# Optimization experiments

Hardware: AMD Instinct MI355X
Metric: run time of the kernel (lower is better)

Reference implementation:

```python
import jax, jax.numpy as jnp
from jax import lax
import numpy as np

DN = ('NCHW', 'OIHW', 'NCHW')
LEAKY_SLOPE = 0.01  # torch nn.LeakyReLU default


def conv(x, w, b=None, stride=1, pad=0):
    y = lax.conv_general_dilated(x, w, (stride, stride), [(pad, pad), (pad, pad)],
                                 dimension_numbers=DN)
    return y if b is None else y + b[None, :, None, None]


def conv_transpose2d(x, w, b):
    # torch ConvTranspose2d(k=4, s=2, p=1); w layout (Cin, Cout, 4, 4)
    wf = jnp.transpose(jnp.flip(w, (2, 3)), (1, 0, 2, 3))  # -> OIHW
    y = lax.conv_general_dilated(x, wf, (1, 1), [(2, 2), (2, 2)],
                                 lhs_dilation=(2, 2), dimension_numbers=DN)
    return y + b[None, :, None, None]


def residual_stack(x, rw3, rw1):
    # 6 ResidualLayers: x + conv1x1(relu(conv3x3(x))), both convs bias-free
    for i in range(rw3.shape[0]):
        h = jax.nn.relu(conv(x, rw3[i], pad=1))
        x = x + conv(h, rw1[i])
    return x


def vector_quantize(latents, codebook):
    # latents: [B, D, H, W] -> NHWC
    lat = jnp.transpose(latents, (0, 2, 3, 1))
    B, H, W, D = lat.shape
    flat = lat.reshape(-1, D)  # [N, D]
    # pairwise squared distances [N, K]
    dist = (jnp.sum(flat ** 2, axis=1, keepdims=True)
            + jnp.sum(codebook ** 2, axis=1)
            - 2.0 * flat @ codebook.T)
    inds = jnp.argmin(dist, axis=1)            # [N]
    q = codebook[inds].reshape(B, H, W, D)     # gather == one-hot matmul
    commitment_loss = jnp.mean((lax.stop_gradient(q) - lat) ** 2)
    embedding_loss = jnp.mean((q - lax.stop_gradient(lat)) ** 2)
    q_st = lat + lax.stop_gradient(q - lat)    # straight-through
    return jnp.transpose(q_st, (0, 3, 1, 2)), embedding_loss, commitment_loss


def setup_inputs() -> dict:
    key = jax.random.key(0)
    ks = iter(jax.random.split(key, 32))
    B, C, S = 16, 3, 128
    H0, H1 = 128, 256          # hidden_dims
    D, K = 64, 512             # embedding_dim, num_embeddings
    n_res = 6

    def w(shape, scale=0.05):
        return (jax.random.normal(next(ks), shape, dtype=jnp.float32) * scale)

    inp = {
        'x': jax.random.normal(next(ks), (B, C, S, S), dtype=jnp.float32),
        # encoder
        'ew0': w((H0, C, 4, 4)), 'eb0': jnp.zeros((H0,), jnp.float32),
        'ew1': w((H1, H0, 4, 4)), 'eb1': jnp.zeros((H1,), jnp.float32),
        'ew2': w((H1, H1, 3, 3)), 'eb2': jnp.zeros((H1,), jnp.float32),
        'erw3': w((n_res, H1, H1, 3, 3)),
        'erw1': w((n_res, H1, H1, 1, 1)),
        'ew3': w((D, H1, 1, 1)), 'eb3': jnp.zeros((D,), jnp.float32),
        # codebook, uniform(-1/K, 1/K) as in torch init
        'codebook': jax.random.uniform(next(ks), (K, D), jnp.float32, -1.0 / K, 1.0 / K),
        # decoder
        'dw0': w((H1, D, 3, 3)), 'db0': jnp.zeros((H1,), jnp.float32),
        'drw3': w((n_res, H1, H1, 3, 3)),
        'drw1': w((n_res, H1, H1, 1, 1)),
        'tw0': w((H1, H0, 4, 4)), 'tb0': jnp.zeros((H0,), jnp.float32),
        'tw1': w((H0, C, 4, 4)), 'tb1': jnp.zeros((C,), jnp.float32),
    }
    return inp


def reference(x, ew0, eb0, ew1, eb1, ew2, eb2, erw3, erw1, ew3, eb3,
              codebook, dw0, db0, drw3, drw1, tw0, tb0, tw1, tb1):
    lrelu = lambda t: jax.nn.leaky_relu(t, LEAKY_SLOPE)
    # encoder: two stride-2 downsamples, conv3x3, 6 residuals, 1x1 -> D
    h = lrelu(conv(x, ew0, eb0, stride=2, pad=1))   # [B,128,64,64]
    h = lrelu(conv(h, ew1, eb1, stride=2, pad=1))   # [B,256,32,32]
    h = lrelu(conv(h, ew2, eb2, stride=1, pad=1))
    h = residual_stack(h, erw3, erw1)
    h = lrelu(h)
    z = lrelu(conv(h, ew3, eb3))                    # [B,64,32,32]
    # vector quantization
    q, embedding_loss, commitment_loss = vector_quantize(z, codebook)
    # decoder
    d = lrelu(conv(q, dw0, db0, stride=1, pad=1))   # [B,256,32,32]
    d = residual_stack(d, drw3, drw1)
    d = lrelu(d)
    d = lrelu(conv_transpose2d(d, tw0, tb0))        # [B,128,64,64]
    recons = jnp.tanh(conv_transpose2d(d, tw1, tb1))  # [B,3,128,128]
    return recons, embedding_loss, commitment_loss
```

## Files before the change

kernel.cpp:

```cpp
#include <hip/hip_runtime.h>
#include <math.h>


typedef __attribute__((ext_vector_type(8))) short bf16x8;
typedef __attribute__((ext_vector_type(4))) float f32x4;

__device__ __forceinline__ float bf2f(short s) {
    unsigned u = ((unsigned)(unsigned short)s) << 16;
    return __builtin_bit_cast(float, u);
}
__device__ __forceinline__ unsigned short f2bfu(float f) {
    unsigned u = __builtin_bit_cast(unsigned, f);
    u = (u + 0x7fff + ((u >> 16) & 1)) >> 16;
    return (unsigned short)u;
}
__device__ __forceinline__ short f2bf(float f) { return (short)f2bfu(f); }
__device__ __forceinline__ int pack2(float a, float b) {
    return (int)f2bfu(a) | ((int)f2bfu(b) << 16);
}

template<int ACT>
__device__ __forceinline__ float actf(float v) {
    if (ACT == 1) return fmaxf(v, 0.f);
    if (ACT == 2) return v > 0.f ? v : 0.01f * v;
    return v;
}

__device__ __forceinline__ void gload_lds16(const void* g, void* l) {
    __builtin_amdgcn_global_load_lds(
        (const __attribute__((address_space(1))) unsigned int*)g,
        (__attribute__((address_space(3))) unsigned int*)l, 16, 0, 0);
}

__device__ __forceinline__ int fof(int r) { return (r & 3) ^ ((r >> 2) & 3); }

#define WAITV(N) asm volatile("s_waitcnt vmcnt(" #N ")" ::: "memory")
#define LGKM0 asm volatile("s_waitcnt lgkmcnt(0)" ::: "memory")

__global__ __launch_bounds__(256) void prep_perm_k(const float* __restrict__ src,
        short* __restrict__ dst, int COUT, int CIN, int T, int total) {
    int i = blockIdx.x * 256 + threadIdx.x;
    if (i >= total) return;
    int ic = i % CIN; int r = i / CIN;
    int oc = r % COUT; r /= COUT;
    int t = r % T; int c = r / T;
    dst[i] = f2bf(src[(((size_t)c * COUT + oc) * CIN + ic) * T + t]);
}

__global__ __launch_bounds__(256) void prep_tw0_k(const float* __restrict__ src,
        short* __restrict__ dst) {
    int i = blockIdx.x * 256 + threadIdx.x;
    if (i >= 4 * 4 * 128 * 256) return;
    int ic = i & 255; int r = i >> 8;
    int oc = r & 127; r >>= 7;
    int tap = r & 3; int par = r >> 2;
    int py = par >> 1, px = par & 1, my = tap >> 1, mx = tap & 1;
    int ky = 2 * my + (py ^ 1), kx = 2 * mx + (px ^ 1);
    dst[i] = f2bf(src[(((size_t)ic * 128 + oc) * 4 + ky) * 4 + kx]);
}

__global__ __launch_bounds__(256) void halo_zero_k(short* __restrict__ p,
        int W, int C) {
    int row = blockIdx.x, img = blockIdx.y;
    short* base = p + ((size_t)img * W + row) * W * C;
    bool full = (row < 2) || (row >= W - 2);
    int n = full ? W * C : 4 * C;
    for (int t = threadIdx.x * 8; t < n; t += 256 * 8) {
        int off = t;
        if (!full) off = (t < 2 * C) ? t : (W - 2) * C + (t - 2 * C);
        *(int4*)(base + off) = int4{0, 0, 0, 0};
    }
}

template<int CIN, int NTAPS, int TAPPAT, int SM, int INW, int OUTACT,
         bool HASB, bool FUSE>
__global__ __launch_bounds__(512, 1) void rconv_k(
        const short* __restrict__ in, const short* __restrict__ Wp,
        const float* __restrict__ bias, const short* __restrict__ W1p,
        short* __restrict__ outp) {
    constexpr int CH64 = (CIN >= 128) ? CIN / 64 : 1;
    constexpr int LG2 = (CH64 == 4) ? 2 : (CH64 == 2) ? 1 : 0;
    constexpr int ST = NTAPS * CH64;
    __shared__ short sLds[FUSE ? 81920 : 61440];
    const int tid = threadIdx.x;
    const int lane = tid & 63, wv = tid >> 6;
    const int wc = wv & 3, kg = wv >> 2;
    const int pix0 = blockIdx.x * 64;
    const int l15 = lane & 15, hi = lane >> 4;
    const int sl = (hi ^ fof(l15)) * 8;

    const int arow = (tid >> 2) & 63, akk = tid >> 8, aslot = tid & 3;
    const short* Aptr;
    {
        int pixa = pix0 + arow;
        int ba = pixa >> 10, Ya = (pixa >> 5) & 31, Xa = pixa & 31;
        Aptr = in + (size_t)((ba * INW + SM * Ya + 2) * INW + (SM * Xa + 2)) * CIN
                  + akk * 32 + (aslot ^ fof(arow)) * 8;
    }
    const short* Bptr[4];
#pragma unroll
    for (int j = 0; j < 4; j++) {
        int gb = tid + 512 * j;
        int kkb = gb >> 10, oc = (gb >> 2) & 255, slb = gb & 3;
        Bptr[j] = Wp + (size_t)oc * CIN + kkb * 32 + ((slb ^ fof(oc)) * 8);
    }

    auto stage = [&](int s, int bi) {
        int t = s >> LG2;
        int c0 = (s & (CH64 - 1)) * 64;
        int rof, cof;
        if (TAPPAT == 1) { rof = t / 3 - 1; cof = t % 3 - 1; }
        else             { rof = (t >> 2) - 1; cof = (t & 3) - 1; }
        int aoff = (rof * INW + cof) * CIN + c0;
        int woff = t * (256 * CIN) + c0;
        char* L = (char*)sLds + bi * 40960;
        gload_lds16(Aptr + aoff, L + tid * 16);
#pragma unroll
        for (int j = 0; j < 4; j++)
            gload_lds16(Bptr[j] + woff, L + 8192 + (tid + 512 * j) * 16);
    };

    f32x4 acc[4][4];
#pragma unroll
    for (int mi = 0; mi < 4; mi++)
#pragma unroll
        for (int ni = 0; ni < 4; ni++) acc[mi][ni] = f32x4{0.f, 0.f, 0.f, 0.f};

    stage(0, 0);
    stage(1, 1);
    int bi = 0;
    for (int s = 0; s < ST; ++s) {
        if (s < ST - 1) { WAITV(5); } else { WAITV(0); }
        __builtin_amdgcn_s_barrier();
        int nx = bi + 2; if (nx >= 3) nx -= 3;
        if (s + 2 < ST) stage(s + 2, nx);
        const short* LA = sLds + bi * 20480 + kg * 2048;
        const short* LB = sLds + bi * 20480 + 4096 + kg * 8192;
        bf16x8 af[4], bfr[4];
#pragma unroll
        for (int mi = 0; mi < 4; mi++)
            af[mi] = *(const bf16x8*)(LA + (mi * 16 + l15) * 32 + sl);
#pragma unroll
        for (int ni = 0; ni < 4; ni++)
            bfr[ni] = *(const bf16x8*)(LB + (wc * 64 + ni * 16 + l15) * 32 + sl);
        __builtin_amdgcn_s_setprio(1);
#pragma unroll
        for (int mi = 0; mi < 4; mi++)
#pragma unroll
            for (int ni = 0; ni < 4; ni++)
                acc[mi][ni] = __builtin_amdgcn_mfma_f32_16x16x32_bf16(
                    af[mi], bfr[ni], acc[mi][ni], 0, 0, 0);
        __builtin_amdgcn_s_setprio(0);
        bi = (bi == 2) ? 0 : bi + 1;
    }

    float* MB = (float*)sLds;

    const short* W1ptr[4];
    if (FUSE) {
#pragma unroll
        for (int j = 0; j < 4; j++) {
            int gb = tid + 512 * j;
            int kkb = gb >> 10, oc = (gb >> 2) & 255, slb = gb & 3;
            W1ptr[j] = W1p + (size_t)oc * 256 + kkb * 32 + ((slb ^ fof(oc)) * 8);
        }
    }
    auto stage2 = [&](int c) {
        char* L = (char*)sLds + 65536 + (c & 1) * 32768;
#pragma unroll
        for (int j = 0; j < 4; j++)
            gload_lds16(W1ptr[j] + c * 64, L + (tid + 512 * j) * 16);
    };

    __syncthreads();
    if (FUSE) { stage2(0); stage2(1); }
    if (kg == 1) {
#pragma unroll
        for (int mi = 0; mi < 4; mi++)
#pragma unroll
            for (int ni = 0; ni < 4; ni++)
#pragma unroll
                for (int r = 0; r < 4; r++)
                    MB[(mi * 16 + hi * 4 + r) * 256 + wc * 64 + ni * 16 + l15]
                        = acc[mi][ni][r];
    }
    __syncthreads();

    if (!FUSE) {
        if (kg == 0) {
#pragma unroll
            for (int mi = 0; mi < 4; mi++)
#pragma unroll
                for (int ni = 0; ni < 4; ni++) {
                    int col = wc * 64 + ni * 16 + l15;
                    float b = HASB ? bias[col] : 0.f;
#pragma unroll
                    for (int r = 0; r < 4; r++) {
                        int row = mi * 16 + hi * 4 + r;
                        MB[row * 256 + col] += acc[mi][ni][r] + b;
                    }
                }
        }
        __syncthreads();
#pragma unroll
        for (int j = 0; j < 4; j++) {
            int idx = j * 512 + tid;
            int p = idx >> 5, c0 = (idx & 31) * 8;
            int pix = pix0 + p;
            int b = pix >> 10, Y = (pix >> 5) & 31, X = pix & 31;
            size_t base = (((size_t)b * 36 + Y + 2) * 36 + X + 2) * 256 + c0;
            const float4* m4 = (const float4*)(MB + idx * 8);
            float4 lo = m4[0], hv = m4[1];
            int pk[4];
            pk[0] = pack2(actf<OUTACT>(lo.x), actf<OUTACT>(lo.y));
            pk[1] = pack2(actf<OUTACT>(lo.z), actf<OUTACT>(lo.w));
            pk[2] = pack2(actf<OUTACT>(hv.x), actf<OUTACT>(hv.y));
            pk[3] = pack2(actf<OUTACT>(hv.z), actf<OUTACT>(hv.w));
            *(int4*)(outp + base) = *(int4*)pk;
        }
        return;
    }

    short* H = sLds + 65536;
    if (kg == 0) {
#pragma unroll
        for (int mi = 0; mi < 4; mi++)
#pragma unroll
            for (int ni = 0; ni < 4; ni++) {
                int col = wc * 64 + ni * 16 + l15;
#pragma unroll
                for (int r = 0; r < 4; r++) {
                    int row = mi * 16 + hi * 4 + r;
                    float v = acc[mi][ni][r] + MB[row * 256 + col];
                    H[((col >> 5) * 64 + row) * 32
                      + (((col >> 3) & 3) ^ fof(row)) * 8 + (col & 7)]
                        = f2bf(fmaxf(v, 0.f));
                }
            }
    }
    __syncthreads();

    f32x4 acc2[4][4];
#pragma unroll
    for (int mi = 0; mi < 4; mi++)
#pragma unroll
        for (int ni = 0; ni < 4; ni++) acc2[mi][ni] = f32x4{0.f, 0.f, 0.f, 0.f};

    for (int s2 = 0; s2 < 4; ++s2) {
        if (s2 < 3) { WAITV(4); } else { WAITV(0); }
        __builtin_amdgcn_s_barrier();
        const short* HB = H + (s2 * 2 + kg) * 2048;
        const short* LW = sLds + 32768 + (s2 & 1) * 16384 + kg * 8192;
        bf16x8 af2[4], bf2r[4];
#pragma unroll
        for (int mi = 0; mi < 4; mi++)
            af2[mi] = *(const bf16x8*)(HB + (mi * 16 + l15) * 32 + sl);
#pragma unroll
        for (int ni = 0; ni < 4; ni++)
            bf2r[ni] = *(const bf16x8*)(LW + (wc * 64 + ni * 16 + l15) * 32 + sl);
        LGKM0;
        __builtin_amdgcn_sched_barrier(0);
        __builtin_amdgcn_s_barrier();
        if (s2 < 2) stage2(s2 + 2);
        __builtin_amdgcn_s_setprio(1);
#pragma unroll
        for (int mi = 0; mi < 4; mi++)
#pragma unroll
            for (int ni = 0; ni < 4; ni++)
                acc2[mi][ni] = __builtin_amdgcn_mfma_f32_16x16x32_bf16(
                    af2[mi], bf2r[ni], acc2[mi][ni], 0, 0, 0);
        __builtin_amdgcn_s_setprio(0);
    }

    __syncthreads();
    if (kg == 1) {
#pragma unroll
        for (int mi = 0; mi < 4; mi++)
#pragma unroll
            for (int ni = 0; ni < 4; ni++)
#pragma unroll
                for (int r = 0; r < 4; r++)
                    MB[(mi * 16 + hi * 4 + r) * 256 + wc * 64 + ni * 16 + l15]
                        = acc2[mi][ni][r];
    }
    __syncthreads();
    if (kg == 0) {
#pragma unroll
        for (int mi = 0; mi < 4; mi++)
#pragma unroll
            for (int ni = 0; ni < 4; ni++) {
                int col = wc * 64 + ni * 16 + l15;
#pragma unroll
                for (int r = 0; r < 4; r++) {
                    int row = mi * 16 + hi * 4 + r;
                    MB[row * 256 + col] += acc2[mi][ni][r];
                }
            }
    }
    __syncthreads();
#pragma unroll
    for (int j = 0; j < 4; j++) {
        int idx = j * 512 + tid;
        int p = idx >> 5, c0 = (idx & 31) * 8;
        int pix = pix0 + p;
        int b = pix >> 10, Y = (pix >> 5) & 31, X = pix & 31;
        size_t base = (((size_t)b * 36 + Y + 2) * 36 + X + 2) * 256 + c0;
        const float4* m4 = (const float4*)(MB + idx * 8);
        float4 lo = m4[0], hv = m4[1];
        bf16x8 rv = *(const bf16x8*)(in + base);
        int pk[4];
        pk[0] = pack2(actf<OUTACT>(lo.x + bf2f(rv[0])),
                      actf<OUTACT>(lo.y + bf2f(rv[1])));
        pk[1] = pack2(actf<OUTACT>(lo.z + bf2f(rv[2])),
                      actf<OUTACT>(lo.w + bf2f(rv[3])));
        pk[2] = pack2(actf<OUTACT>(hv.x + bf2f(rv[4])),
                      actf<OUTACT>(hv.y + bf2f(rv[5])));
        pk[3] = pack2(actf<OUTACT>(hv.z + bf2f(rv[6])),
                      actf<OUTACT>(hv.w + bf2f(rv[7])));
        *(int4*)(outp + base) = *(int4*)pk;
    }
}

template<int CIN, int COUT, int NTAPS, int TAPPAT, int SM, int INW,
         int OUTACT, bool RES, bool HASB, int OUTMODE, int BN>
__global__ __launch_bounds__(256) void gconv_k(
        const short* __restrict__ in, const short* __restrict__ Wp,
        const float* __restrict__ bias, const short* __restrict__ res,
        void* __restrict__ outp) {
    constexpr int KCH = CIN / 32;
    constexpr int LG = (KCH == 8) ? 3 : (KCH == 4) ? 2 : (KCH == 2) ? 1 : 0;
    constexpr int ST = NTAPS * KCH;
    constexpr int NF = BN / 32;
    constexpr int WN = BN / 2;
    __shared__ short sA[3 * 128 * 32];
    __shared__ short sB[3 * BN * 32];
    const int tid = threadIdx.x;
    const int lane = tid & 63, wv = tid >> 6;
    const int wr = wv >> 1, wc = wv & 1;
    const int pix0 = blockIdx.x * 128;
    const int oc0 = blockIdx.y * BN;
    int py = 0, px = 0;
    if (TAPPAT == 3) {
        int par = blockIdx.z;
        py = par >> 1; px = par & 1;
        Wp += (size_t)par * NTAPS * COUT * CIN;
    }
    const int sp = tid >> 2;
    const int swz = ((tid & 3) ^ fof(sp)) * 8;
    int rbA[2];
#pragma unroll
    for (int rd = 0; rd < 2; rd++) {
        int pix = pix0 + sp + rd * 64;
        int b = pix >> 10, Y = (pix >> 5) & 31, X = pix & 31;
        rbA[rd] = ((b * INW + SM * Y + 2) * INW + (SM * X + 2)) * CIN + swz;
    }
    const int wb0 = (oc0 + sp) * CIN + swz;
    const int wb1 = (oc0 + sp + 64) * CIN + swz;

    f32x4 acc[4][NF];
#pragma unroll
    for (int i = 0; i < 4; i++)
#pragma unroll
        for (int j = 0; j < NF; j++) acc[i][j] = f32x4{0.f, 0.f, 0.f, 0.f};

    const int sslot = ((lane >> 4) ^ fof(lane & 15)) * 8;
    const int abase = (wr * 64 + (lane & 15)) * 32 + sslot;
    const int bbase = (wc * WN + (lane & 15)) * 32 + sslot;

    auto stage = [&](int s, int biq) {
        int t = s >> LG, c = s & (KCH - 1);
        int rof, cof;
        if (TAPPAT == 0) { rof = 0; cof = 0; }
        else if (TAPPAT == 1) { rof = t / 3 - 1; cof = t % 3 - 1; }
        else if (TAPPAT == 2) { rof = t / 4 - 1; cof = t % 4 - 1; }
        else { int my = t >> 1, mx = t & 1;
               rof = (py == 0) ? -my : 1 - my;
               cof = (px == 0) ? -mx : 1 - mx; }
        const int tapoff = (rof * INW + cof) * CIN + c * 32;
        char* a = (char*)sA + biq * 8192;
        char* b = (char*)sB + biq * (BN * 64);
        const short* wt = Wp + (size_t)t * COUT * CIN + c * 32;
        gload_lds16(in + rbA[0] + tapoff, a + tid * 16);
        gload_lds16(in + rbA[1] + tapoff, a + 4096 + tid * 16);
        gload_lds16(wt + wb0, b + tid * 16);
        if (BN == 128) gload_lds16(wt + wb1, b + 4096 + tid * 16);
    };

    stage(0, 0);
    stage(1, 1);
    int cur = 0;
    for (int s = 0; s < ST; ++s) {
        if (s < ST - 1) {
            if (BN == 128) { WAITV(4); } else { WAITV(3); }
        } else {
            WAITV(0);
        }
        __builtin_amdgcn_s_barrier();
        int nxt = cur + 2; if (nxt >= 3) nxt -= 3;
        if (s + 2 < ST) stage(s + 2, nxt);
        const short* a = sA + cur * 4096;
        const short* b = sB + cur * (BN * 32);
        bf16x8 af[4], bfm[NF];
#pragma unroll
        for (int mi = 0; mi < 4; mi++)
            af[mi] = *(const bf16x8*)(a + abase + mi * 512);
#pragma unroll
        for (int ni = 0; ni < NF; ni++)
            bfm[ni] = *(const bf16x8*)(b + bbase + ni * 512);
        __builtin_amdgcn_s_setprio(1);
#pragma unroll
        for (int mi = 0; mi < 4; mi++)
#pragma unroll
            for (int ni = 0; ni < NF; ni++)
                acc[mi][ni] = __builtin_amdgcn_mfma_f32_16x16x32_bf16(
                    af[mi], bfm[ni], acc[mi][ni], 0, 0, 0);
        __builtin_amdgcn_s_setprio(0);
        cur = (cur == 2) ? 0 : cur + 1;
    }
#pragma unroll
    for (int mi = 0; mi < 4; mi++) {
#pragma unroll
        for (int r = 0; r < 4; r++) {
            int pix = pix0 + wr * 64 + mi * 16 + (lane >> 4) * 4 + r;
            int b = pix >> 10, Y = (pix >> 5) & 31, X = pix & 31;
            size_t rowoff = 0;
            if (OUTMODE == 0)
                rowoff = (((size_t)b * 36 + Y + 2) * 36 + X + 2) * COUT;
            else if (OUTMODE == 2)
                rowoff = (((size_t)b * 68 + 2 * Y + py + 2) * 68 + 2 * X + px + 2) * 128;
#pragma unroll
            for (int ni = 0; ni < NF; ni++) {
                int col = oc0 + wc * WN + ni * 16 + (lane & 15);
                float v = acc[mi][ni][r];
                if (HASB) v += bias[col];
                if (OUTMODE == 1) {
                    ((float*)outp)[(size_t)pix * COUT + col] = actf<OUTACT>(v);
                } else {
                    size_t off = rowoff + col;
                    if (RES) v += bf2f(res[off]);
                    ((short*)outp)[off] = f2bf(actf<OUTACT>(v));
                }
            }
        }
    }
}

__global__ __launch_bounds__(256) void conv0_k(const float* __restrict__ x,
        const float* __restrict__ W, const float* __restrict__ bias,
        short* __restrict__ P0) {
    __shared__ float sIn[3 * 4 * 130];
    __shared__ float sW[48 * 4 * 36];
    int y = blockIdx.x, b = blockIdx.y;
    int tid = threadIdx.x;
    for (int t = tid; t < 6144; t += 256) {
        int k = t >> 7, oc = t & 127;
        sW[(k * 4 + (oc >> 5)) * 36 + (oc & 31)] = W[(size_t)oc * 48 + k];
    }
    for (int t = tid; t < 1560; t += 256) {
        int ic = t / 520; int rem = t - ic * 520;
        int ry = rem / 130, rx = rem - ry * 130;
        int iy = 2 * y - 1 + ry, ix = rx - 1;
        float v = 0.f;
        if ((unsigned)iy < 128u && (unsigned)ix < 128u)
            v = x[((size_t)b * 3 + ic) * 16384 + iy * 128 + ix];
        sIn[t] = v;
    }
    __syncthreads();
    int p = tid >> 2, g = tid & 3, oc0 = g * 32;
    float acc[32];
#pragma unroll
    for (int o = 0; o < 32; o++) acc[o] = bias[oc0 + o];
#pragma unroll
    for (int ic = 0; ic < 3; ic++)
#pragma unroll
        for (int ky = 0; ky < 4; ky++) {
            const float* ib = sIn + ic * 520 + ky * 130 + 2 * p;
#pragma unroll
            for (int kx = 0; kx < 4; kx++) {
                float xv = ib[kx];
                const float* wr_ = sW + ((ic * 16 + ky * 4 + kx) * 4 + g) * 36;
#pragma unroll
                for (int q = 0; q < 8; q++) {
                    float4 w = *(const float4*)(wr_ + q * 4);
                    acc[4 * q + 0] += w.x * xv; acc[4 * q + 1] += w.y * xv;
                    acc[4 * q + 2] += w.z * xv; acc[4 * q + 3] += w.w * xv;
                }
            }
        }
    size_t base = (((size_t)b * 68 + y + 2) * 68 + p + 2) * 128 + oc0;
#pragma unroll
    for (int q4 = 0; q4 < 4; q4++) {
        int pk[4];
#pragma unroll
        for (int j = 0; j < 4; j++) {
            float v0 = actf<2>(acc[q4 * 8 + 2 * j]);
            float v1 = actf<2>(acc[q4 * 8 + 2 * j + 1]);
            pk[j] = pack2(v0, v1);
        }
        *(int4*)(P0 + base + q4 * 8) = *(int4*)pk;
    }
}

__global__ __launch_bounds__(256) void vq_argmin_k(const float* __restrict__ zr,
        const float* __restrict__ cb, int* __restrict__ ind) {
    __shared__ short sZ[2][128 * 32];
    __shared__ short sC[2][128 * 32];
    __shared__ float sN[128];
    const int tid = threadIdx.x;
    const int lane = tid & 63, wv = tid >> 6;
    const int pos0 = blockIdx.x * 128;
#pragma unroll
    for (int it = 0; it < 4; ++it) {
        int task = tid + it * 256;
        int row = task >> 3, kq = task & 7;
        const float4* zp = (const float4*)(zr + (size_t)(pos0 + row) * 64 + kq * 8);
        float4 v0 = zp[0], v1 = zp[1];
        int slot = ((kq & 3) ^ fof(row)) * 8;
        short tmp[8] = {f2bf(v0.x), f2bf(v0.y), f2bf(v0.z), f2bf(v0.w),
                        f2bf(v1.x), f2bf(v1.y), f2bf(v1.z), f2bf(v1.w)};
        *(bf16x8*)&sZ[kq >> 2][row * 32 + slot] = *(bf16x8*)tmp;
    }
    const int sslot = ((lane >> 4) ^ fof(lane & 15)) * 8;
    const int l15 = lane & 15;
    float best[2][4]; int bidx[2][4];
#pragma unroll
    for (int mi = 0; mi < 2; mi++)
#pragma unroll
        for (int r = 0; r < 4; r++) { best[mi][r] = INFINITY; bidx[mi][r] = 0; }
    for (int ch = 0; ch < 4; ++ch) {
        __syncthreads();
#pragma unroll
        for (int it = 0; it < 4; ++it) {
            int task = tid + it * 256;
            int row = task >> 3, kq = task & 7;
            const float4* cp = (const float4*)(cb + (size_t)(ch * 128 + row) * 64 + kq * 8);
            float4 v0 = cp[0], v1 = cp[1];
            int slot = ((kq & 3) ^ fof(row)) * 8;
            short tmp[8] = {f2bf(v0.x), f2bf(v0.y), f2bf(v0.z), f2bf(v0.w),
                            f2bf(v1.x), f2bf(v1.y), f2bf(v1.z), f2bf(v1.w)};
            *(bf16x8*)&sC[kq >> 2][row * 32 + slot] = *(bf16x8*)tmp;
        }
        if (tid < 128) {
            const float4* cp = (const float4*)(cb + (size_t)(ch * 128 + tid) * 64);
            float s = 0.f;
#pragma unroll
            for (int q = 0; q < 16; q++) {
                float4 v = cp[q];
                s += v.x * v.x + v.y * v.y + v.z * v.z + v.w * v.w;
            }
            sN[tid] = s;
        }
        __syncthreads();
        f32x4 acc[2][8];
#pragma unroll
        for (int mi = 0; mi < 2; mi++)
#pragma unroll
            for (int ni = 0; ni < 8; ni++) acc[mi][ni] = f32x4{0.f, 0.f, 0.f, 0.f};
#pragma unroll
        for (int kc = 0; kc < 2; ++kc) {
            bf16x8 za[2], ca[8];
#pragma unroll
            for (int mi = 0; mi < 2; mi++)
                za[mi] = *(const bf16x8*)&sZ[kc][(wv * 32 + mi * 16 + l15) * 32 + sslot];
#pragma unroll
            for (int ni = 0; ni < 8; ni++)
                ca[ni] = *(const bf16x8*)&sC[kc][(ni * 16 + l15) * 32 + sslot];
#pragma unroll
            for (int mi = 0; mi < 2; mi++)
#pragma unroll
                for (int ni = 0; ni < 8; ni++)
                    acc[mi][ni] = __builtin_amdgcn_mfma_f32_16x16x32_bf16(
                        za[mi], ca[ni], acc[mi][ni], 0, 0, 0);
        }
#pragma unroll
        for (int mi = 0; mi < 2; mi++)
#pragma unroll
            for (int ni = 0; ni < 8; ni++) {
                float nrm = sN[ni * 16 + l15];
                int idx = ch * 128 + ni * 16 + l15;
#pragma unroll
                for (int r = 0; r < 4; r++) {
                    float sc = nrm - 2.f * acc[mi][ni][r];
                    if (sc < best[mi][r]) { best[mi][r] = sc; bidx[mi][r] = idx; }
                }
            }
    }
#pragma unroll
    for (int m = 1; m < 16; m <<= 1) {
#pragma unroll
        for (int mi = 0; mi < 2; mi++)
#pragma unroll
            for (int r = 0; r < 4; r++) {
                float os = __shfl_xor(best[mi][r], m);
                int   oi = __shfl_xor(bidx[mi][r], m);
                if (os < best[mi][r] || (os == best[mi][r] && oi < bidx[mi][r])) {
                    best[mi][r] = os; bidx[mi][r] = oi;
                }
            }
    }
    if (l15 == 0) {
        int g = lane >> 4;
#pragma unroll
        for (int mi = 0; mi < 2; mi++)
#pragma unroll
            for (int r = 0; r < 4; r++)
                ind[pos0 + wv * 32 + mi * 16 + g * 4 + r] = bidx[mi][r];
    }
}

__global__ __launch_bounds__(256) void vq_gather_k(const float* __restrict__ zr,
        const float* __restrict__ cb, const int* __restrict__ ind,
        short* __restrict__ q, float* __restrict__ part) {
    int pos = blockIdx.x * 256 + threadIdx.x;
    int b = pos >> 10, hw = pos & 1023, y = hw >> 5, xx = hw & 31;
    int idx = ind[pos];
    const float4* cp = (const float4*)(cb + (size_t)idx * 64);
    const float4* zp = (const float4*)(zr + (size_t)pos * 64);
    size_t qb = (((size_t)b * 36 + y + 2) * 36 + xx + 2) * 64;
    float sum = 0.f;
#pragma unroll
    for (int d4 = 0; d4 < 16; d4++) {
        float4 c = cp[d4], z = zp[d4];
        float dx = c.x - z.x, dy = c.y - z.y, dz = c.z - z.z, dw = c.w - z.w;
        sum += dx * dx + dy * dy + dz * dz + dw * dw;
        ((int*)(q + qb))[2 * d4] = pack2(c.x, c.y);
        ((int*)(q + qb))[2 * d4 + 1] = pack2(c.z, c.w);
    }
#pragma unroll
    for (int m = 1; m < 64; m <<= 1) sum += __shfl_xor(sum, m);
    __shared__ float sred[4];
    int lane = threadIdx.x & 63, wvv = threadIdx.x >> 6;
    if (lane == 0) sred[wvv] = sum;
    __syncthreads();
    if (threadIdx.x == 0)
        part[blockIdx.x] = sred[0] + sred[1] + sred[2] + sred[3];
}

__global__ void finalize_k(const float* __restrict__ part, float* __restrict__ out) {
    if (threadIdx.x == 0) {
        float s = 0.f;
        for (int k = 0; k < 64; k++) s += part[k];
        float m = s / 1048576.f;
        out[786432] = m;
        out[786433] = m;
    }
}

__global__ __launch_bounds__(256) void tw1_k(const short* __restrict__ in,
        const float* __restrict__ W, const float* __restrict__ bias,
        float* __restrict__ out) {
    __shared__ float sW[16 * 128 * 4];
    int b = blockIdx.y, y0 = blockIdx.x * 8;
    int tid = threadIdx.x;
    for (int t = tid; t < 2048; t += 256) {
        int k = t >> 7, ic = t & 127;
        float4 v;
        v.x = W[((size_t)ic * 3 + 0) * 16 + k];
        v.y = W[((size_t)ic * 3 + 1) * 16 + k];
        v.z = W[((size_t)ic * 3 + 2) * 16 + k];
        v.w = 0.f;
        *(float4*)&sW[t * 4] = v;
    }
    __syncthreads();
    int r = tid >> 5, g = tid & 31;
    int oy = y0 + r, py = oy & 1, Y = oy >> 1, pxp = g & 1;
    float acc[4][3];
#pragma unroll
    for (int p = 0; p < 4; p++)
#pragma unroll
        for (int o = 0; o < 3; o++) acc[p][o] = 0.f;
#pragma unroll
    for (int my = 0; my < 2; my++) {
        int iy = Y + ((py == 0) ? -my : 1 - my) + 2;
        const short* rowp = in + (((size_t)b * 68 + iy) * 68) * 128;
        int ky = 2 * my + (py ^ 1);
#pragma unroll
        for (int mx = 0; mx < 2; mx++) {
            int kx = 2 * mx + (pxp ^ 1);
            int cof = ((pxp == 0) ? -mx : 1 - mx) + 2;
            const float* wbase = &sW[((ky * 4 + kx) * 128) * 4];
            const short* pptr[4];
#pragma unroll
            for (int p = 0; p < 4; p++) {
                int X = ((g + 32 * p) >> 1) + cof;
                pptr[p] = rowp + (size_t)X * 128;
            }
            for (int icb = 0; icb < 16; icb++) {
                bf16x8 v[4];
#pragma unroll
                for (int p = 0; p < 4; p++)
                    v[p] = *(const bf16x8*)(pptr[p] + icb * 8);
#pragma unroll
                for (int j = 0; j < 8; j++) {
                    float4 w = *(const float4*)&wbase[(icb * 8 + j) * 4];
#pragma unroll
                    for (int p = 0; p < 4; p++) {
                        float xv = bf2f(v[p][j]);
                        acc[p][0] += w.x * xv;
                        acc[p][1] += w.y * xv;
                        acc[p][2] += w.z * xv;
                    }
                }
            }
        }
    }
#pragma unroll
    for (int p = 0; p < 4; p++) {
        int ox = g + 32 * p;
#pragma unroll
        for (int o = 0; o < 3; o++)
            out[(((size_t)b * 3 + o) << 14) + oy * 128 + ox] =
                tanhf(acc[p][o] + bias[o]);
    }
}

extern "C" void kernel_launch(void* const* d_in, const int* in_sizes, int n_in,
                              void* d_out, int out_size, void* d_ws, size_t ws_size,
                              hipStream_t stream) {
    const float* x    = (const float*)d_in[0];
    const float* ew0  = (const float*)d_in[1];
    const float* eb0  = (const float*)d_in[2];
    const float* ew1  = (const float*)d_in[3];
    const float* eb1  = (const float*)d_in[4];
    const float* ew2  = (const float*)d_in[5];
    const float* eb2  = (const float*)d_in[6];
    const float* erw3 = (const float*)d_in[7];
    const float* erw1 = (const float*)d_in[8];
    const float* ew3  = (const float*)d_in[9];
    const float* eb3  = (const float*)d_in[10];
    const float* cbk  = (const float*)d_in[11];
    const float* dw0  = (const float*)d_in[12];
    const float* db0  = (const float*)d_in[13];
    const float* drw3 = (const float*)d_in[14];
    const float* drw1 = (const float*)d_in[15];
    const float* tw0  = (const float*)d_in[16];
    const float* tb0  = (const float*)d_in[17];
    const float* tw1  = (const float*)d_in[18];
    const float* tb1  = (const float*)d_in[19];
    float* out = (float*)d_out;

    short* S = (short*)d_ws;
    short* P0  = S;
    short* PB  = P0 + 9469952;
    short* PC  = PB + 5308416;
    short* Pq  = PC + 5308416;
    short* Wp1 = Pq + 1327104;
    short* We2 = Wp1 + 524288;
    short* Wer3 = We2 + 589824;
    short* We11 = Wer3 + 3538944;
    short* Wz   = We11 + 393216;
    short* Wd0  = Wz + 16384;
    short* Wdr3 = Wd0 + 147456;
    short* Wdr1 = Wdr3 + 3538944;
    short* Wt0  = Wdr1 + 393216;
    float* F   = (float*)(S + 31080448);
    float* Zr  = F;
    float* PART = Zr + 1048576;
    int*   IND = (int*)(PART + 64);

    halo_zero_k<<<dim3(68, 16), 256, 0, stream>>>(P0, 68, 128);
    halo_zero_k<<<dim3(36, 16), 256, 0, stream>>>(PB, 36, 256);
    halo_zero_k<<<dim3(36, 16), 256, 0, stream>>>(PC, 36, 256);
    halo_zero_k<<<dim3(36, 16), 256, 0, stream>>>(Pq, 36, 64);

    auto gp = [](int n) { return dim3((n + 255) / 256); };
    prep_perm_k<<<gp(524288), 256, 0, stream>>>(ew1, Wp1, 256, 128, 16, 524288);
    prep_perm_k<<<gp(589824), 256, 0, stream>>>(ew2, We2, 256, 256, 9, 589824);
    prep_perm_k<<<gp(3538944), 256, 0, stream>>>(erw3, Wer3, 256, 256, 9, 3538944);
    prep_perm_k<<<gp(393216), 256, 0, stream>>>(erw1, We11, 256, 256, 1, 393216);
    prep_perm_k<<<gp(16384), 256, 0, stream>>>(ew3, Wz, 64, 256, 1, 16384);
    prep_perm_k<<<gp(147456), 256, 0, stream>>>(dw0, Wd0, 256, 64, 9, 147456);
    prep_perm_k<<<gp(3538944), 256, 0, stream>>>(drw3, Wdr3, 256, 256, 9, 3538944);
    prep_perm_k<<<gp(393216), 256, 0, stream>>>(drw1, Wdr1, 256, 256, 1, 393216);
    prep_tw0_k<<<gp(524288), 256, 0, stream>>>(tw0, Wt0);

    conv0_k<<<dim3(64, 16), 256, 0, stream>>>(x, ew0, eb0, P0);
    rconv_k<128, 16, 2, 2, 68, 2, true, false>
        <<<256, 512, 0, stream>>>(P0, Wp1, eb1, nullptr, PB);
    rconv_k<256, 9, 1, 1, 36, 2, true, false>
        <<<256, 512, 0, stream>>>(PB, We2, eb2, nullptr, PC);
    for (int i = 0; i < 6; i++) {
        short* inb  = (i & 1) ? PB : PC;
        short* outb = (i & 1) ? PC : PB;
        if (i < 5)
            rconv_k<256, 9, 1, 1, 36, 0, false, true>
                <<<256, 512, 0, stream>>>(inb, Wer3 + (size_t)i * 589824,
                    nullptr, We11 + (size_t)i * 65536, outb);
        else
            rconv_k<256, 9, 1, 1, 36, 2, false, true>
                <<<256, 512, 0, stream>>>(inb, Wer3 + (size_t)i * 589824,
                    nullptr, We11 + (size_t)i * 65536, outb);
    }
    gconv_k<256, 64, 1, 0, 1, 36, 2, false, true, 1, 64>
        <<<dim3(128, 1), 256, 0, stream>>>(PC, Wz, eb3, nullptr, Zr);

    vq_argmin_k<<<128, 256, 0, stream>>>(Zr, cbk, IND);
    vq_gather_k<<<64, 256, 0, stream>>>(Zr, cbk, IND, Pq, PART);

    rconv_k<64, 9, 1, 1, 36, 2, true, false>
        <<<256, 512, 0, stream>>>(Pq, Wd0, db0, nullptr, PC);
    for (int i = 0; i < 6; i++) {
        short* inb  = (i & 1) ? PB : PC;
        short* outb = (i & 1) ? PC : PB;
        if (i < 5)
            rconv_k<256, 9, 1, 1, 36, 0, false, true>
                <<<256, 512, 0, stream>>>(inb, Wdr3 + (size_t)i * 589824,
                    nullptr, Wdr1 + (size_t)i * 65536, outb);
        else
            rconv_k<256, 9, 1, 1, 36, 2, false, true>
                <<<256, 512, 0, stream>>>(inb, Wdr3 + (size_t)i * 589824,
                    nullptr, Wdr1 + (size_t)i * 65536, outb);
    }
    gconv_k<256, 128, 4, 3, 1, 36, 2, false, true, 2, 128>
        <<<dim3(128, 1, 4), 256, 0, stream>>>(PC, Wt0, tb0, nullptr, P0);
    tw1_k<<<dim3(16, 16), 256, 0, stream>>>(P0, tw1, tb1, out);

    finalize_k<<<1, 64, 0, stream>>>(PART, out);
}
```

Baseline: 628.8 us.

## Deepen conv pipeline to four LDS stages and merge weight-prep launches

The implicit-GEMM conv kernel moves from a 3-buffer to a 4-buffer LDS ring with three stages in flight, adjusting vmcnt waits and relocating the fused 1x1 weight and hidden buffers to fit. LDS is now always 160KB, even for non-fused variants. Separately, nine weight permutation/conversion launches are merged into one kernel with block-range dispatch to cut launch overhead. The deeper prefetch is meant to hide global-load latency, at the cost of more LDS per block.

```diff
diff --git a/kernel.cpp b/kernel.cpp
--- a/kernel.cpp
+++ b/kernel.cpp
@@ -35,11 +35,9 @@
 __device__ __forceinline__ int fof(int r) { return (r & 3) ^ ((r >> 2) & 3); }
 
 #define WAITV(N) asm volatile("s_waitcnt vmcnt(" #N ")" ::: "memory")
-#define LGKM0 asm volatile("s_waitcnt lgkmcnt(0)" ::: "memory")
-
-__global__ __launch_bounds__(256) void prep_perm_k(const float* __restrict__ src,
-        short* __restrict__ dst, int COUT, int CIN, int T, int total) {
-    int i = blockIdx.x * 256 + threadIdx.x;
+
+__device__ __forceinline__ void perm_one(const float* src, short* dst,
+        int COUT, int CIN, int T, int i, int total) {
     if (i >= total) return;
     int ic = i % CIN; int r = i / CIN;
     int oc = r % COUT; r /= COUT;
@@ -47,16 +45,40 @@
     dst[i] = f2bf(src[(((size_t)c * COUT + oc) * CIN + ic) * T + t]);
 }
 
-__global__ __launch_bounds__(256) void prep_tw0_k(const float* __restrict__ src,
-        short* __restrict__ dst) {
-    int i = blockIdx.x * 256 + threadIdx.x;
-    if (i >= 4 * 4 * 128 * 256) return;
-    int ic = i & 255; int r = i >> 8;
-    int oc = r & 127; r >>= 7;
-    int tap = r & 3; int par = r >> 2;
-    int py = par >> 1, px = par & 1, my = tap >> 1, mx = tap & 1;
-    int ky = 2 * my + (py ^ 1), kx = 2 * mx + (px ^ 1);
-    dst[i] = f2bf(src[(((size_t)ic * 128 + oc) * 4 + ky) * 4 + kx]);
+__global__ __launch_bounds__(256) void prep_all_k(
+        const float* ew1, const float* ew2, const float* erw3,
+        const float* erw1, const float* ew3, const float* dw0,
+        const float* drw3, const float* drw1, const float* tw0,
+        short* Wp1, short* We2, short* Wer3, short* We11, short* Wz,
+        short* Wd0, short* Wdr3, short* Wdr1, short* Wt0) {
+    int bid = blockIdx.x, tid = threadIdx.x;
+    if (bid < 2048) {
+        perm_one(ew1, Wp1, 256, 128, 16, bid * 256 + tid, 524288);
+    } else if (bid < 4352) {
+        perm_one(ew2, We2, 256, 256, 9, (bid - 2048) * 256 + tid, 589824);
+    } else if (bid < 18176) {
+        perm_one(erw3, Wer3, 256, 256, 9, (bid - 4352) * 256 + tid, 3538944);
+    } else if (bid < 19712) {
+        perm_one(erw1, We11, 256, 256, 1, (bid - 18176) * 256 + tid, 393216);
+    } else if (bid < 19776) {
+        perm_one(ew3, Wz, 64, 256, 1, (bid - 19712) * 256 + tid, 16384);
+    } else if (bid < 20352) {
+        perm_one(dw0, Wd0, 256, 64, 9, (bid - 19776) * 256 + tid, 147456);
+    } else if (bid < 34176) {
+        perm_one(drw3, Wdr3, 256, 256, 9, (bid - 20352) * 256 + tid, 3538944);
+    } else if (bid < 35712) {
+        perm_one(drw1, Wdr1, 256, 256, 1, (bid - 34176) * 256 + tid, 393216);
+    } else {
+        int i = (bid - 35712) * 256 + tid;
+        if (i < 524288) {
+            int ic = i & 255; int r = i >> 8;
+            int oc = r & 127; r >>= 7;
+            int tap = r & 3; int par = r >> 2;
+            int py = par >> 1, px = par & 1, my = tap >> 1, mx = tap & 1;
+            int ky = 2 * my + (py ^ 1), kx = 2 * mx + (px ^ 1);
+            Wt0[i] = f2bf(tw0[(((size_t)ic * 128 + oc) * 4 + ky) * 4 + kx]);
+        }
+    }
 }
 
 __global__ __launch_bounds__(256) void halo_zero_k(short* __restrict__ p,
@@ -81,7 +103,7 @@
     constexpr int CH64 = (CIN >= 128) ? CIN / 64 : 1;
     constexpr int LG2 = (CH64 == 4) ? 2 : (CH64 == 2) ? 1 : 0;
     constexpr int ST = NTAPS * CH64;
-    __shared__ short sLds[FUSE ? 81920 : 61440];
+    __shared__ short sLds[81920];
     const int tid = threadIdx.x;
     const int lane = tid & 63, wv = tid >> 6;
     const int wc = wv & 3, kg = wv >> 2;
@@ -128,12 +150,14 @@
 
     stage(0, 0);
     stage(1, 1);
+    stage(2, 2);
     int bi = 0;
     for (int s = 0; s < ST; ++s) {
-        if (s < ST - 1) { WAITV(5); } else { WAITV(0); }
+        if (s < ST - 2)      { WAITV(10); }
+        else if (s == ST - 2){ WAITV(5); }
+        else                 { WAITV(0); }
         __builtin_amdgcn_s_barrier();
-        int nx = bi + 2; if (nx >= 3) nx -= 3;
-        if (s + 2 < ST) stage(s + 2, nx);
+        if (s + 3 < ST) stage(s + 3, (bi + 3) & 3);
         const short* LA = sLds + bi * 20480 + kg * 2048;
         const short* LB = sLds + bi * 20480 + 4096 + kg * 8192;
         bf16x8 af[4], bfr[4];
@@ -151,7 +175,7 @@
                 acc[mi][ni] = __builtin_amdgcn_mfma_f32_16x16x32_bf16(
                     af[mi], bfr[ni], acc[mi][ni], 0, 0, 0);
         __builtin_amdgcn_s_setprio(0);
-        bi = (bi == 2) ? 0 : bi + 1;
+        bi = (bi + 1) & 3;
     }
 
     float* MB = (float*)sLds;
@@ -166,7 +190,7 @@
         }
     }
     auto stage2 = [&](int c) {
-        char* L = (char*)sLds + 65536 + (c & 1) * 32768;
+        char* L = (char*)sLds + 98304 + (c & 1) * 32768;
 #pragma unroll
         for (int j = 0; j < 4; j++)
             gload_lds16(W1ptr[j] + c * 64, L + (tid + 512 * j) * 16);
@@ -221,7 +245,7 @@
         return;
     }
 
-    short* H = sLds + 65536;
+    short* H = sLds + 32768;
     if (kg == 0) {
 #pragma unroll
         for (int mi = 0; mi < 4; mi++)
@@ -250,7 +274,7 @@
         if (s2 < 3) { WAITV(4); } else { WAITV(0); }
         __builtin_amdgcn_s_barrier();
         const short* HB = H + (s2 * 2 + kg) * 2048;
-        const short* LW = sLds + 32768 + (s2 & 1) * 16384 + kg * 8192;
+        const short* LW = sLds + 49152 + (s2 & 1) * 16384 + kg * 8192;
         bf16x8 af2[4], bf2r[4];
 #pragma unroll
         for (int mi = 0; mi < 4; mi++)
@@ -258,7 +282,7 @@
 #pragma unroll
         for (int ni = 0; ni < 4; ni++)
             bf2r[ni] = *(const bf16x8*)(LW + (wc * 64 + ni * 16 + l15) * 32 + sl);
-        LGKM0;
+        asm volatile("s_waitcnt lgkmcnt(0)" ::: "memory");
         __builtin_amdgcn_sched_barrier(0);
         __builtin_amdgcn_s_barrier();
         if (s2 < 2) stage2(s2 + 2);
@@ -763,16 +787,8 @@
     halo_zero_k<<<dim3(36, 16), 256, 0, stream>>>(PC, 36, 256);
     halo_zero_k<<<dim3(36, 16), 256, 0, stream>>>(Pq, 36, 64);
 
-    auto gp = [](int n) { return dim3((n + 255) / 256); };
-    prep_perm_k<<<gp(524288), 256, 0, stream>>>(ew1, Wp1, 256, 128, 16, 524288);
-    prep_perm_k<<<gp(589824), 256, 0, stream>>>(ew2, We2, 256, 256, 9, 589824);
-    prep_perm_k<<<gp(3538944), 256, 0, stream>>>(erw3, Wer3, 256, 256, 9, 3538944);
-    prep_perm_k<<<gp(393216), 256, 0, stream>>>(erw1, We11, 256, 256, 1, 393216);
-    prep_perm_k<<<gp(16384), 256, 0, stream>>>(ew3, Wz, 64, 256, 1, 16384);
-    prep_perm_k<<<gp(147456), 256, 0, stream>>>(dw0, Wd0, 256, 64, 9, 147456);
-    prep_perm_k<<<gp(3538944), 256, 0, stream>>>(drw3, Wdr3, 256, 256, 9, 3538944);
-    prep_perm_k<<<gp(393216), 256, 0, stream>>>(drw1, Wdr1, 256, 256, 1, 393216);
-    prep_tw0_k<<<gp(524288), 256, 0, stream>>>(tw0, Wt0);
+    prep_all_k<<<37760, 256, 0, stream>>>(ew1, ew2, erw3, erw1, ew3, dw0,
+        drw3, drw1, tw0, Wp1, We2, Wer3, We11, Wz, Wd0, Wdr3, Wdr1, Wt0);
 
     conv0_k<<<dim3(64, 16), 256, 0, stream>>>(x, ew0, eb0, P0);
     rconv_k<128, 16, 2, 2, 68, 2, true, false>
```

Result: no change. 621.3 us (-1.2%).
